# Optimization experiments

Measured on AMD Instinct MI355X. Metric: run time of the kernel, lower is better.

Reference implementation:

```python
import jax, jax.numpy as jnp
import numpy as np

EMB = 1024
HEADS = 16
HEAD_DIM = EMB // HEADS


def setup_inputs() -> dict:
    key = jax.random.key(0)
    ks = jax.random.split(key, 6)
    B, S = 4, 1024
    inputs = jax.random.normal(ks[0], (B, S, EMB), dtype=jnp.float32)
    # causal mask: 1.0 where attention is disallowed (added * -1e9 in the layer)
    mask = (1.0 - jnp.tril(jnp.ones((S, S), dtype=jnp.float32)))[None, None, :, :]
    scale = 1.0 / np.sqrt(EMB)
    wq = jax.random.normal(ks[1], (EMB, EMB), dtype=jnp.float32) * scale
    wk = jax.random.normal(ks[2], (EMB, EMB), dtype=jnp.float32) * scale
    wv = jax.random.normal(ks[3], (EMB, EMB), dtype=jnp.float32) * scale
    wo = jax.random.normal(ks[4], (EMB, EMB), dtype=jnp.float32) * scale
    zb = jnp.zeros((EMB,), dtype=jnp.float32)
    return {"inputs": inputs, "mask": mask, "wq": wq, "bq": zb, "wk": wk,
            "bk": zb, "wv": wv, "bv": zb, "wo": wo, "bo": zb}


def _split_heads(t, B):
    # [B, S, E] -> [B, H, S, Dh]
    return t.reshape(B, -1, HEADS, HEAD_DIM).transpose(0, 2, 1, 3)


def reference(inputs, mask, wq, bq, wk, bk, wv, bv, wo, bo):
    B = inputs.shape[0]
    q = _split_heads(inputs @ wq + bq, B)
    k = _split_heads(inputs @ wk + bk, B)
    v = _split_heads(inputs @ wv + bv, B)
    # NOTE: source divides by sqrt(sqrt(head_num)) = head_num**0.25
    scores = jnp.einsum('bhsd,bhtd->bhst', q, k) / jnp.asarray(HEADS, inputs.dtype) ** 0.25
    if mask is not None:
        scores = scores + mask * -1e9
    attn = jax.nn.softmax(scores, axis=-1)
    z = jnp.einsum('bhst,bhtd->bhsd', attn, v)
    # Faithful to source: reshape [B,H,S,Dh] -> [B,S,E] WITHOUT transposing heads back
    z = z.reshape(B, -1, EMB)
    return z @ wo + bo
```

## Files before the change

### kernel.cpp

```cpp
#include <hip/hip_runtime.h>
#include <hip/hip_bf16.h>
#include <stdint.h>

typedef __attribute__((ext_vector_type(8))) short short8;
typedef __attribute__((ext_vector_type(4))) float float4v;

#define SEQ   1024
#define NQKV  3072

__device__ __forceinline__ float bf2f(ushort h) {
    union { uint u; float f; } c; c.u = ((uint)h) << 16; return c.f;
}
__device__ __forceinline__ ushort f2bf(float f) {
    union { uint u; float f; } c; c.f = f;
    uint u = c.u;
    return (ushort)((u + 0x7fffu + ((u >> 16) & 1u)) >> 16);
}
__device__ __forceinline__ void gl2lds16(const ushort* g, ushort* l) {
    __builtin_amdgcn_global_load_lds(
        (const __attribute__((address_space(1))) unsigned int*)(g),
        (__attribute__((address_space(3))) unsigned int*)(l),
        16, 0, 0);
}

__global__ void detect_k(const uint* __restrict__ x, int* __restrict__ flag) {
    __shared__ int cnt[256];
    int h = 0;
    for (int i = threadIdx.x; i < 4096; i += 256) {
        uint w = x[i];
        uint e = (w >> 7) & 0xFFu;
        h += (e >= 100u && e <= 130u) ? 1 : 0;
    }
    cnt[threadIdx.x] = h;
    __syncthreads();
    if (threadIdx.x == 0) {
        int s = 0;
        for (int i = 0; i < 256; i++) s += cnt[i];
        flag[0] = (s > 2048) ? 0 : 1;
    }
}

__global__ __launch_bounds__(256) void xcvt_k(const void* __restrict__ x,
                                              ushort* __restrict__ xc,
                                              const int* __restrict__ flag) {
    int i = (blockIdx.x * 256 + threadIdx.x) * 4;
    if (*flag) {
        const float* xf = (const float*)x;
        float4 v = *(const float4*)(xf + i);
        ushort4 o;
        o.x = f2bf(v.x); o.y = f2bf(v.y); o.z = f2bf(v.z); o.w = f2bf(v.w);
        *(ushort4*)(xc + i) = o;
    } else {
        *(ushort4*)(xc + i) = *(const ushort4*)((const ushort*)x + i);
    }
}

__global__ void biascat_k(const void* __restrict__ bq, const void* __restrict__ bk,
                          const void* __restrict__ bv, const void* __restrict__ bo,
                          const int* __restrict__ flag, ushort* __restrict__ bout) {
    int i = blockIdx.x * 256 + threadIdx.x;
    int sel = i >> 10, j = i & 1023;
    const void* p = (sel == 0) ? bq : (sel == 1) ? bk : (sel == 2) ? bv : bo;
    bout[i] = (*flag) ? f2bf(((const float*)p)[j]) : ((const ushort*)p)[j];
}

__global__ __launch_bounds__(256) void transpose4_k(const void* __restrict__ w0,
                                                    const void* __restrict__ w1,
                                                    const void* __restrict__ w2,
                                                    const void* __restrict__ w3,
                                                    ushort* __restrict__ outall,
                                                    const int* __restrict__ flag) {
    __shared__ ushort tile[64][72];
    int z = blockIdx.z;
    const void* in = (z == 0) ? w0 : (z == 1) ? w1 : (z == 2) ? w2 : w3;
    ushort* out = outall + (size_t)z * 1024 * 1024;
    int k0 = blockIdx.x * 64;
    int n0 = blockIdx.y * 64;
    int t = threadIdx.x;
    int r = t >> 3, c = (t & 7) * 8;
    bool isf = (*flag != 0);
#pragma unroll
    for (int p = 0; p < 2; p++) {
        int rr = r + p * 32;
        if (isf) {
            const float* src = (const float*)in + (size_t)(k0 + rr) * 1024 + n0 + c;
            float4 v0 = *(const float4*)src;
            float4 v1 = *(const float4*)(src + 4);
            tile[rr][c + 0] = f2bf(v0.x); tile[rr][c + 1] = f2bf(v0.y);
            tile[rr][c + 2] = f2bf(v0.z); tile[rr][c + 3] = f2bf(v0.w);
            tile[rr][c + 4] = f2bf(v1.x); tile[rr][c + 5] = f2bf(v1.y);
            tile[rr][c + 6] = f2bf(v1.z); tile[rr][c + 7] = f2bf(v1.w);
        } else {
            uint4 v = *(const uint4*)((const ushort*)in + (size_t)(k0 + rr) * 1024 + n0 + c);
            *(uint4*)&tile[rr][c] = v;
        }
    }
    __syncthreads();
#pragma unroll
    for (int p = 0; p < 2; p++) {
        int n = r + p * 32;
        ushort vals[8];
#pragma unroll
        for (int j = 0; j < 8; j++) vals[j] = tile[c + j][n];
        *(uint4*)(out + (size_t)(n0 + n) * 1024 + k0 + c) = *(uint4*)vals;
    }
}

__global__ __launch_bounds__(256) void vtrans_k(const ushort* __restrict__ qkv,
                                                ushort* __restrict__ vt) {
    __shared__ ushort tile[64][72];
    int t0 = blockIdx.x * 64;
    int bh = blockIdx.y;
    int b = bh >> 4, h = bh & 15;
    int t = threadIdx.x;
    int r = t >> 3, c = (t & 7) * 8;
#pragma unroll
    for (int p = 0; p < 2; p++) {
        int rr = r + p * 32;
        uint4 v = *(const uint4*)(qkv + (size_t)(b * 1024 + t0 + rr) * NQKV + 2048 + h * 64 + c);
        *(uint4*)&tile[rr][c] = v;
    }
    __syncthreads();
#pragma unroll
    for (int p = 0; p < 2; p++) {
        int d = r + p * 32;
        ushort vals[8];
#pragma unroll
        for (int j = 0; j < 8; j++) vals[j] = tile[c + j][d];
        *(uint4*)(vt + ((size_t)bh * 64 + d) * 1024 + t0 + c) = *(uint4*)vals;
    }
}

template <bool DUAL>
__global__ __launch_bounds__(256) void gemm128_k(const ushort* __restrict__ A,
                                                 const ushort* __restrict__ BT,
                                                 const ushort* __restrict__ bias,
                                                 void* __restrict__ C,
                                                 const int* __restrict__ flag,
                                                 int M, int N, int K) {
    __shared__ ushort As[128 * 32];
    __shared__ ushort Bs[128 * 32];
    int n0 = blockIdx.x * 128, m0 = blockIdx.y * 128;
    int t = threadIdx.x;
    int w = t >> 6, lane = t & 63, q = lane >> 4, ln = lane & 15;
    int wr = w >> 1, wc = w & 1;

    float4v acc[4][4];
#pragma unroll
    for (int r = 0; r < 4; r++)
#pragma unroll
        for (int cc = 0; cc < 4; cc++) acc[r][cc] = (float4v){0.f, 0.f, 0.f, 0.f};

    for (int k0 = 0; k0 < K; k0 += 32) {
#pragma unroll
        for (int j = 0; j < 2; j++) {
            int c = j * 256 + t;
            int row = c >> 2, s = c & 3;
            int kc = s ^ ((row >> 1) & 3);
            gl2lds16(A + (size_t)(m0 + row) * K + k0 + kc * 8, &As[c * 8]);
            gl2lds16(BT + (size_t)(n0 + row) * K + k0 + kc * 8, &Bs[c * 8]);
        }
        __syncthreads();
        short8 af[4], bf[4];
#pragma unroll
        for (int r = 0; r < 4; r++) {
            int row = wr * 64 + r * 16 + ln;
            af[r] = *(const short8*)&As[((row << 2) | (q ^ ((row >> 1) & 3))) * 8];
            int col = wc * 64 + r * 16 + ln;
            bf[r] = *(const short8*)&Bs[((col << 2) | (q ^ ((col >> 1) & 3))) * 8];
        }
#pragma unroll
        for (int r = 0; r < 4; r++)
#pragma unroll
            for (int cc = 0; cc < 4; cc++)
                acc[r][cc] = __builtin_amdgcn_mfma_f32_16x16x32_bf16(af[r], bf[cc], acc[r][cc], 0, 0, 0);
        __syncthreads();
    }

    bool outf = DUAL && (*flag != 0);
#pragma unroll
    for (int cc = 0; cc < 4; cc++) {
        int n = n0 + wc * 64 + cc * 16 + ln;
        float bs = bf2f(bias[n]);
#pragma unroll
        for (int r = 0; r < 4; r++) {
#pragma unroll
            for (int i = 0; i < 4; i++) {
                int m = m0 + wr * 64 + r * 16 + q * 4 + i;
                float v = acc[r][cc][i] + bs;
                if (outf) ((float*)C)[(size_t)m * N + n] = v;
                else      ((ushort*)C)[(size_t)m * N + n] = f2bf(v);
            }
        }
    }
}

__global__ __launch_bounds__(256) void attn_k(const ushort* __restrict__ qkv,
                                              const ushort* __restrict__ vt,
                                              ushort* __restrict__ zp) {
    __shared__ ushort Ks[64 * 72];
    __shared__ ushort Vs[64 * 72];
    __shared__ ushort P[4][16 * 76];
    int pr = blockIdx.x;
    int bh = blockIdx.y;
    int b = bh >> 4, h = bh & 15;
    int t = threadIdx.x;
    int w = t >> 6, lane = t & 63, q = lane >> 4, ln = lane & 15;

    const ushort* Qp = qkv + (size_t)(b * SEQ) * NQKV + h * 64;
    const ushort* Kp = qkv + (size_t)(b * SEQ) * NQKV + 1024 + h * 64;
    const ushort* Vt = vt + (size_t)bh * 64 * 1024;

    int srr = t >> 3;
    int scol = (t & 7) * 8;

    for (int rep = 0; rep < 2; rep++) {
        int ti = rep ? (15 - pr) : pr;
        int s0 = ti * 64, sw = s0 + w * 16;

        short8 aq0 = *(const short8*)(Qp + (size_t)(sw + ln) * NQKV + q * 8);
        short8 aq1 = *(const short8*)(Qp + (size_t)(sw + ln) * NQKV + 32 + q * 8);

        float m_i[4], l_i[4];
        float4v o[4];
#pragma unroll
        for (int i = 0; i < 4; i++) { m_i[i] = -__builtin_inff(); l_i[i] = 0.f; }
#pragma unroll
        for (int nb = 0; nb < 4; nb++) o[nb] = (float4v){0.f, 0.f, 0.f, 0.f};

        for (int kt = 0; kt <= ti; kt++) {
            int t0 = kt * 64;
            __syncthreads();
#pragma unroll
            for (int p2 = 0; p2 < 2; p2++) {
                int r = srr + p2 * 32;
                *(uint4*)&Ks[r * 72 + scol] = *(const uint4*)(Kp + (size_t)(t0 + r) * NQKV + scol);
                *(uint4*)&Vs[r * 72 + scol] = *(const uint4*)(Vt + (size_t)r * 1024 + t0 + scol);
            }
            __syncthreads();

            float4v s[4];
#pragma unroll
            for (int nb = 0; nb < 4; nb++) s[nb] = (float4v){0.f, 0.f, 0.f, 0.f};
#pragma unroll
            for (int nb = 0; nb < 4; nb++) {
                short8 kf0 = *(const short8*)&Ks[(nb * 16 + ln) * 72 + q * 8];
                short8 kf1 = *(const short8*)&Ks[(nb * 16 + ln) * 72 + 32 + q * 8];
                s[nb] = __builtin_amdgcn_mfma_f32_16x16x32_bf16(aq0, kf0, s[nb], 0, 0, 0);
                s[nb] = __builtin_amdgcn_mfma_f32_16x16x32_bf16(aq1, kf1, s[nb], 0, 0, 0);
            }
            float sc[4][4];
#pragma unroll
            for (int nb = 0; nb < 4; nb++)
#pragma unroll
                for (int i = 0; i < 4; i++) {
                    int srow = sw + q * 4 + i;
                    int col = t0 + nb * 16 + ln;
                    sc[nb][i] = (col <= srow) ? s[nb][i] * 0.5f : -1e30f;
                }
            float p[4][4];
#pragma unroll
            for (int i = 0; i < 4; i++) {
                float bm = fmaxf(fmaxf(sc[0][i], sc[1][i]), fmaxf(sc[2][i], sc[3][i]));
#pragma unroll
                for (int mk = 1; mk < 16; mk <<= 1) bm = fmaxf(bm, __shfl_xor(bm, mk, 64));
                float mn = fmaxf(m_i[i], bm);
                float alpha = __expf(m_i[i] - mn);
                float sum = 0.f;
#pragma unroll
                for (int nb = 0; nb < 4; nb++) {
                    p[nb][i] = __expf(sc[nb][i] - mn);
                    sum += p[nb][i];
                }
#pragma unroll
                for (int mk = 1; mk < 16; mk <<= 1) sum += __shfl_xor(sum, mk, 64);
                l_i[i] = l_i[i] * alpha + sum;
                m_i[i] = mn;
#pragma unroll
                for (int nb = 0; nb < 4; nb++) o[nb][i] *= alpha;
            }
#pragma unroll
            for (int nb = 0; nb < 4; nb++)
#pragma unroll
                for (int i = 0; i < 4; i++)
                    P[w][(q * 4 + i) * 76 + nb * 16 + ln] = f2bf(p[nb][i]);
            asm volatile("s_waitcnt lgkmcnt(0)\n" ::: "memory");
            short8 ap0 = *(const short8*)&P[w][ln * 76 + q * 8];
            short8 ap1 = *(const short8*)&P[w][ln * 76 + 32 + q * 8];
#pragma unroll
            for (int nb = 0; nb < 4; nb++) {
                short8 bv0 = *(const short8*)&Vs[(nb * 16 + ln) * 72 + q * 8];
                short8 bv1 = *(const short8*)&Vs[(nb * 16 + ln) * 72 + 32 + q * 8];
                o[nb] = __builtin_amdgcn_mfma_f32_16x16x32_bf16(ap0, bv0, o[nb], 0, 0, 0);
                o[nb] = __builtin_amdgcn_mfma_f32_16x16x32_bf16(ap1, bv1, o[nb], 0, 0, 0);
            }
        }

#pragma unroll
        for (int nb = 0; nb < 4; nb++) {
#pragma unroll
            for (int i = 0; i < 4; i++) {
                int srow = sw + q * 4 + i;
                int d = nb * 16 + ln;
                float z = o[nb][i] / l_i[i];
                int sp = h * 64 + (srow >> 4);
                int ep = ((srow & 15) << 6) + d;
                zp[((size_t)(b * SEQ + sp)) * 1024 + ep] = f2bf(z);
            }
        }
    }
}

extern "C" void kernel_launch(void* const* d_in, const int* in_sizes, int n_in,
                              void* d_out, int out_size, void* d_ws, size_t ws_size,
                              hipStream_t stream) {
    const void* X  = d_in[0];
    const void* wq = d_in[2];
    const void* bq = d_in[3];
    const void* wk = d_in[4];
    const void* bk = d_in[5];
    const void* wv = d_in[6];
    const void* bv = d_in[7];
    const void* wo = d_in[8];
    const void* bo = d_in[9];

    char* ws = (char*)d_ws;
    int*    flag  = (int*)ws;
    ushort* biasq = (ushort*)(ws + 4096);
    ushort* WTall = (ushort*)(ws + 12288);
    ushort* Xc    = (ushort*)(ws + 8400896);
    ushort* QKV   = (ushort*)(ws + 16789504);
    ushort* VT    = (ushort*)(ws + 41955328);
    ushort* WTo   = WTall + 3 * 1024 * 1024;
    ushort* ZP    = Xc;

    detect_k<<<1, 256, 0, stream>>>((const uint*)X, flag);
    xcvt_k<<<4096, 256, 0, stream>>>(X, Xc, flag);
    biascat_k<<<16, 256, 0, stream>>>(bq, bk, bv, bo, flag, biasq);
    transpose4_k<<<dim3(16, 16, 4), 256, 0, stream>>>(wq, wk, wv, wo, WTall, flag);
    gemm128_k<false><<<dim3(24, 32), 256, 0, stream>>>(Xc, WTall, biasq, QKV, flag, 4096, NQKV, 1024);
    vtrans_k<<<dim3(16, 64), 256, 0, stream>>>(QKV, VT);
    attn_k<<<dim3(8, 64), 256, 0, stream>>>(QKV, VT, ZP);
    gemm128_k<true><<<dim3(8, 32), 256, 0, stream>>>(ZP, WTo, biasq + 3072, d_out, flag, 4096, 1024, 1024);
}
```

Measured before the change: 214.2 us.

## Use direct global-to-LDS loads with XOR swizzle and one query tile per block

The attention kernel now stages K and V tiles with global_load_lds 16-byte direct copies into an XOR-swizzled unpadded LDS layout, instead of loading into registers and then storing to padded LDS. The paired-tile loop (pr and 15-pr) is removed: each block handles one query tile, with heaviest tiles launched first, which doubles the grid. The causal mask is applied only on the diagonal tile. These target register staging cost, LDS bank conflicts and per-block work imbalance, at the cost of losing the balanced pairing and relying on the runtime to schedule the uneven blocks.

```diff
diff --git a/kernel.cpp b/kernel.cpp
--- a/kernel.cpp
+++ b/kernel.cpp
@@ -198,58 +198,61 @@
 __global__ __launch_bounds__(256) void attn_k(const ushort* __restrict__ qkv,
                                               const ushort* __restrict__ vt,
                                               ushort* __restrict__ zp) {
-    __shared__ ushort Ks[64 * 72];
-    __shared__ ushort Vs[64 * 72];
+    __shared__ ushort Ks[64 * 64];
+    __shared__ ushort Vs[64 * 64];
     __shared__ ushort P[4][16 * 76];
-    int pr = blockIdx.x;
+    int ti = 15 - blockIdx.x;
     int bh = blockIdx.y;
     int b = bh >> 4, h = bh & 15;
     int t = threadIdx.x;
     int w = t >> 6, lane = t & 63, q = lane >> 4, ln = lane & 15;
+    int sw = ti * 64 + w * 16;
 
     const ushort* Qp = qkv + (size_t)(b * SEQ) * NQKV + h * 64;
     const ushort* Kp = qkv + (size_t)(b * SEQ) * NQKV + 1024 + h * 64;
     const ushort* Vt = vt + (size_t)bh * 64 * 1024;
 
-    int srr = t >> 3;
-    int scol = (t & 7) * 8;
-
-    for (int rep = 0; rep < 2; rep++) {
-        int ti = rep ? (15 - pr) : pr;
-        int s0 = ti * 64, sw = s0 + w * 16;
-
-        short8 aq0 = *(const short8*)(Qp + (size_t)(sw + ln) * NQKV + q * 8);
-        short8 aq1 = *(const short8*)(Qp + (size_t)(sw + ln) * NQKV + 32 + q * 8);
-
-        float m_i[4], l_i[4];
-        float4v o[4];
-#pragma unroll
-        for (int i = 0; i < 4; i++) { m_i[i] = -__builtin_inff(); l_i[i] = 0.f; }
-#pragma unroll
-        for (int nb = 0; nb < 4; nb++) o[nb] = (float4v){0.f, 0.f, 0.f, 0.f};
-
-        for (int kt = 0; kt <= ti; kt++) {
-            int t0 = kt * 64;
-            __syncthreads();
-#pragma unroll
-            for (int p2 = 0; p2 < 2; p2++) {
-                int r = srr + p2 * 32;
-                *(uint4*)&Ks[r * 72 + scol] = *(const uint4*)(Kp + (size_t)(t0 + r) * NQKV + scol);
-                *(uint4*)&Vs[r * 72 + scol] = *(const uint4*)(Vt + (size_t)r * 1024 + t0 + scol);
-            }
-            __syncthreads();
-
-            float4v s[4];
-#pragma unroll
-            for (int nb = 0; nb < 4; nb++) s[nb] = (float4v){0.f, 0.f, 0.f, 0.f};
-#pragma unroll
-            for (int nb = 0; nb < 4; nb++) {
-                short8 kf0 = *(const short8*)&Ks[(nb * 16 + ln) * 72 + q * 8];
-                short8 kf1 = *(const short8*)&Ks[(nb * 16 + ln) * 72 + 32 + q * 8];
-                s[nb] = __builtin_amdgcn_mfma_f32_16x16x32_bf16(aq0, kf0, s[nb], 0, 0, 0);
-                s[nb] = __builtin_amdgcn_mfma_f32_16x16x32_bf16(aq1, kf1, s[nb], 0, 0, 0);
-            }
-            float sc[4][4];
+    short8 aq0 = *(const short8*)(Qp + (size_t)(sw + ln) * NQKV + q * 8);
+    short8 aq1 = *(const short8*)(Qp + (size_t)(sw + ln) * NQKV + 32 + q * 8);
+
+    float m_i[4], l_i[4];
+    float4v o[4];
+#pragma unroll
+    for (int i = 0; i < 4; i++) { m_i[i] = -__builtin_inff(); l_i[i] = 0.f; }
+#pragma unroll
+    for (int nb = 0; nb < 4; nb++) o[nb] = (float4v){0.f, 0.f, 0.f, 0.f};
+
+    int rA = ln;
+    for (int kt = 0; kt <= ti; kt++) {
+        int t0 = kt * 64;
+        __syncthreads();
+#pragma unroll
+        for (int j = 0; j < 2; j++) {
+            int c = j * 256 + t;
+            int row = c >> 3, s = c & 7;
+            int kc = s ^ (row & 7);
+            gl2lds16(Kp + (size_t)(t0 + row) * NQKV + kc * 8, &Ks[c * 8]);
+            gl2lds16(Vt + (size_t)row * 1024 + t0 + kc * 8, &Vs[c * 8]);
+        }
+        __syncthreads();
+
+        float4v s[4];
+#pragma unroll
+        for (int nb = 0; nb < 4; nb++) {
+            int row = nb * 16 + rA;
+            short8 kf0 = *(const short8*)&Ks[((row << 3) | (q ^ (row & 7))) * 8];
+            short8 kf1 = *(const short8*)&Ks[((row << 3) | ((4 + q) ^ (row & 7))) * 8];
+            s[nb] = (float4v){0.f, 0.f, 0.f, 0.f};
+            s[nb] = __builtin_amdgcn_mfma_f32_16x16x32_bf16(aq0, kf0, s[nb], 0, 0, 0);
+            s[nb] = __builtin_amdgcn_mfma_f32_16x16x32_bf16(aq1, kf1, s[nb], 0, 0, 0);
+        }
+        float sc[4][4];
+        if (kt < ti) {
+#pragma unroll
+            for (int nb = 0; nb < 4; nb++)
+#pragma unroll
+                for (int i = 0; i < 4; i++) sc[nb][i] = s[nb][i] * 0.5f;
+        } else {
 #pragma unroll
             for (int nb = 0; nb < 4; nb++)
 #pragma unroll
@@ -258,55 +261,56 @@
                     int col = t0 + nb * 16 + ln;
                     sc[nb][i] = (col <= srow) ? s[nb][i] * 0.5f : -1e30f;
                 }
-            float p[4][4];
-#pragma unroll
-            for (int i = 0; i < 4; i++) {
-                float bm = fmaxf(fmaxf(sc[0][i], sc[1][i]), fmaxf(sc[2][i], sc[3][i]));
-#pragma unroll
-                for (int mk = 1; mk < 16; mk <<= 1) bm = fmaxf(bm, __shfl_xor(bm, mk, 64));
-                float mn = fmaxf(m_i[i], bm);
-                float alpha = __expf(m_i[i] - mn);
-                float sum = 0.f;
-#pragma unroll
-                for (int nb = 0; nb < 4; nb++) {
-                    p[nb][i] = __expf(sc[nb][i] - mn);
-                    sum += p[nb][i];
-                }
-#pragma unroll
-                for (int mk = 1; mk < 16; mk <<= 1) sum += __shfl_xor(sum, mk, 64);
-                l_i[i] = l_i[i] * alpha + sum;
-                m_i[i] = mn;
-#pragma unroll
-                for (int nb = 0; nb < 4; nb++) o[nb][i] *= alpha;
+        }
+        float p[4][4];
+#pragma unroll
+        for (int i = 0; i < 4; i++) {
+            float bm = fmaxf(fmaxf(sc[0][i], sc[1][i]), fmaxf(sc[2][i], sc[3][i]));
+#pragma unroll
+            for (int mk = 1; mk < 16; mk <<= 1) bm = fmaxf(bm, __shfl_xor(bm, mk, 64));
+            float mn = fmaxf(m_i[i], bm);
+            float alpha = __expf(m_i[i] - mn);
+            float sum = 0.f;
+#pragma unroll
+            for (int nb = 0; nb < 4; nb++) {
+                p[nb][i] = __expf(sc[nb][i] - mn);
+                sum += p[nb][i];
             }
 #pragma unroll
-            for (int nb = 0; nb < 4; nb++)
-#pragma unroll
-                for (int i = 0; i < 4; i++)
-                    P[w][(q * 4 + i) * 76 + nb * 16 + ln] = f2bf(p[nb][i]);
-            asm volatile("s_waitcnt lgkmcnt(0)\n" ::: "memory");
-            short8 ap0 = *(const short8*)&P[w][ln * 76 + q * 8];
-            short8 ap1 = *(const short8*)&P[w][ln * 76 + 32 + q * 8];
-#pragma unroll
-            for (int nb = 0; nb < 4; nb++) {
-                short8 bv0 = *(const short8*)&Vs[(nb * 16 + ln) * 72 + q * 8];
-                short8 bv1 = *(const short8*)&Vs[(nb * 16 + ln) * 72 + 32 + q * 8];
-                o[nb] = __builtin_amdgcn_mfma_f32_16x16x32_bf16(ap0, bv0, o[nb], 0, 0, 0);
-                o[nb] = __builtin_amdgcn_mfma_f32_16x16x32_bf16(ap1, bv1, o[nb], 0, 0, 0);
-            }
-        }
-
+            for (int mk = 1; mk < 16; mk <<= 1) sum += __shfl_xor(sum, mk, 64);
+            l_i[i] = l_i[i] * alpha + sum;
+            m_i[i] = mn;
+#pragma unroll
+            for (int nb = 0; nb < 4; nb++) o[nb][i] *= alpha;
+        }
+#pragma unroll
+        for (int nb = 0; nb < 4; nb++)
+#pragma unroll
+            for (int i = 0; i < 4; i++)
+                P[w][(q * 4 + i) * 76 + nb * 16 + ln] = f2bf(p[nb][i]);
+        asm volatile("s_waitcnt lgkmcnt(0)\n" ::: "memory");
+        short8 ap0 = *(const short8*)&P[w][ln * 76 + q * 8];
+        short8 ap1 = *(const short8*)&P[w][ln * 76 + 32 + q * 8];
 #pragma unroll
         for (int nb = 0; nb < 4; nb++) {
-#pragma unroll
-            for (int i = 0; i < 4; i++) {
-                int srow = sw + q * 4 + i;
-                int d = nb * 16 + ln;
-                float z = o[nb][i] / l_i[i];
-                int sp = h * 64 + (srow >> 4);
-                int ep = ((srow & 15) << 6) + d;
-                zp[((size_t)(b * SEQ + sp)) * 1024 + ep] = f2bf(z);
-            }
+            int row = nb * 16 + rA;
+            short8 bv0 = *(const short8*)&Vs[((row << 3) | (q ^ (row & 7))) * 8];
+            short8 bv1 = *(const short8*)&Vs[((row << 3) | ((4 + q) ^ (row & 7))) * 8];
+            o[nb] = __builtin_amdgcn_mfma_f32_16x16x32_bf16(ap0, bv0, o[nb], 0, 0, 0);
+            o[nb] = __builtin_amdgcn_mfma_f32_16x16x32_bf16(ap1, bv1, o[nb], 0, 0, 0);
+        }
+    }
+
+#pragma unroll
+    for (int nb = 0; nb < 4; nb++) {
+#pragma unroll
+        for (int i = 0; i < 4; i++) {
+            int srow = sw + q * 4 + i;
+            int d = nb * 16 + ln;
+            float z = o[nb][i] / l_i[i];
+            int sp = h * 64 + (srow >> 4);
+            int ep = ((srow & 15) << 6) + d;
+            zp[((size_t)(b * SEQ + sp)) * 1024 + ep] = f2bf(z);
         }
     }
 }
@@ -340,6 +344,6 @@
     transpose4_k<<<dim3(16, 16, 4), 256, 0, stream>>>(wq, wk, wv, wo, WTall, flag);
     gemm128_k<false><<<dim3(24, 32), 256, 0, stream>>>(Xc, WTall, biasq, QKV, flag, 4096, NQKV, 1024);
     vtrans_k<<<dim3(16, 64), 256, 0, stream>>>(QKV, VT);
-    attn_k<<<dim3(8, 64), 256, 0, stream>>>(QKV, VT, ZP);
+    attn_k<<<dim3(16, 64), 256, 0, stream>>>(QKV, VT, ZP);
     gemm128_k<true><<<dim3(8, 32), 256, 0, stream>>>(ZP, WTo, biasq + 3072, d_out, flag, 4096, 1024, 1024);
 }
```

New measurement: 229.4 us. 1.07x slower.

## Double-buffer attention K/V tiles with async global-to-LDS loads and XOR swizzle

Applied to the files above, without the earlier changes.

The attention kernel now stages K and V tiles into two LDS buffers using direct global-to-LDS loads. The next tile is prefetched while the current one is consumed, replacing the synchronous load-store-barrier sequence. The LDS layout drops row padding in favour of an XOR swizzle on 16-byte chunks to avoid bank conflicts. The causal mask is now applied only on the diagonal tile. This costs twice the K/V LDS footprint and depends on the barrier draining outstanding async loads before a buffer is read.

```diff
diff --git a/kernel.cpp b/kernel.cpp
--- a/kernel.cpp
+++ b/kernel.cpp
@@ -198,8 +198,8 @@
 __global__ __launch_bounds__(256) void attn_k(const ushort* __restrict__ qkv,
                                               const ushort* __restrict__ vt,
                                               ushort* __restrict__ zp) {
-    __shared__ ushort Ks[64 * 72];
-    __shared__ ushort Vs[64 * 72];
+    __shared__ ushort Ks[2][64 * 64];
+    __shared__ ushort Vs[2][64 * 64];
     __shared__ ushort P[4][16 * 76];
     int pr = blockIdx.x;
     int bh = blockIdx.y;
@@ -211,12 +211,15 @@
     const ushort* Kp = qkv + (size_t)(b * SEQ) * NQKV + 1024 + h * 64;
     const ushort* Vt = vt + (size_t)bh * 64 * 1024;
 
-    int srr = t >> 3;
-    int scol = (t & 7) * 8;
+    int c0 = t, c1 = 256 + t;
+    int row0 = c0 >> 3, kc0 = (c0 & 7) ^ (row0 & 7);
+    int row1 = c1 >> 3, kc1 = (c1 & 7) ^ (row1 & 7);
 
     for (int rep = 0; rep < 2; rep++) {
         int ti = rep ? (15 - pr) : pr;
-        int s0 = ti * 64, sw = s0 + w * 16;
+        int sw = ti * 64 + w * 16;
+
+        __syncthreads();
 
         short8 aq0 = *(const short8*)(Qp + (size_t)(sw + ln) * NQKV + q * 8);
         short8 aq1 = *(const short8*)(Qp + (size_t)(sw + ln) * NQKV + 32 + q * 8);
@@ -228,36 +231,49 @@
 #pragma unroll
         for (int nb = 0; nb < 4; nb++) o[nb] = (float4v){0.f, 0.f, 0.f, 0.f};
 
+        gl2lds16(Kp + (size_t)row0 * NQKV + kc0 * 8, &Ks[0][c0 * 8]);
+        gl2lds16(Vt + (size_t)row0 * 1024 + kc0 * 8, &Vs[0][c0 * 8]);
+        gl2lds16(Kp + (size_t)row1 * NQKV + kc1 * 8, &Ks[0][c1 * 8]);
+        gl2lds16(Vt + (size_t)row1 * 1024 + kc1 * 8, &Vs[0][c1 * 8]);
+
         for (int kt = 0; kt <= ti; kt++) {
+            int cur = kt & 1;
             int t0 = kt * 64;
             __syncthreads();
-#pragma unroll
-            for (int p2 = 0; p2 < 2; p2++) {
-                int r = srr + p2 * 32;
-                *(uint4*)&Ks[r * 72 + scol] = *(const uint4*)(Kp + (size_t)(t0 + r) * NQKV + scol);
-                *(uint4*)&Vs[r * 72 + scol] = *(const uint4*)(Vt + (size_t)r * 1024 + t0 + scol);
-            }
-            __syncthreads();
+            if (kt < ti) {
+                int nt0 = t0 + 64, nxt = cur ^ 1;
+                gl2lds16(Kp + (size_t)(nt0 + row0) * NQKV + kc0 * 8, &Ks[nxt][c0 * 8]);
+                gl2lds16(Vt + (size_t)row0 * 1024 + nt0 + kc0 * 8, &Vs[nxt][c0 * 8]);
+                gl2lds16(Kp + (size_t)(nt0 + row1) * NQKV + kc1 * 8, &Ks[nxt][c1 * 8]);
+                gl2lds16(Vt + (size_t)row1 * 1024 + nt0 + kc1 * 8, &Vs[nxt][c1 * 8]);
+            }
 
             float4v s[4];
 #pragma unroll
-            for (int nb = 0; nb < 4; nb++) s[nb] = (float4v){0.f, 0.f, 0.f, 0.f};
-#pragma unroll
             for (int nb = 0; nb < 4; nb++) {
-                short8 kf0 = *(const short8*)&Ks[(nb * 16 + ln) * 72 + q * 8];
-                short8 kf1 = *(const short8*)&Ks[(nb * 16 + ln) * 72 + 32 + q * 8];
+                int row = nb * 16 + ln;
+                short8 kf0 = *(const short8*)&Ks[cur][((row << 3) | (q ^ (row & 7))) * 8];
+                short8 kf1 = *(const short8*)&Ks[cur][((row << 3) | ((4 + q) ^ (row & 7))) * 8];
+                s[nb] = (float4v){0.f, 0.f, 0.f, 0.f};
                 s[nb] = __builtin_amdgcn_mfma_f32_16x16x32_bf16(aq0, kf0, s[nb], 0, 0, 0);
                 s[nb] = __builtin_amdgcn_mfma_f32_16x16x32_bf16(aq1, kf1, s[nb], 0, 0, 0);
             }
             float sc[4][4];
-#pragma unroll
-            for (int nb = 0; nb < 4; nb++)
-#pragma unroll
-                for (int i = 0; i < 4; i++) {
-                    int srow = sw + q * 4 + i;
-                    int col = t0 + nb * 16 + ln;
-                    sc[nb][i] = (col <= srow) ? s[nb][i] * 0.5f : -1e30f;
-                }
+            if (kt < ti) {
+#pragma unroll
+                for (int nb = 0; nb < 4; nb++)
+#pragma unroll
+                    for (int i = 0; i < 4; i++) sc[nb][i] = s[nb][i] * 0.5f;
+            } else {
+#pragma unroll
+                for (int nb = 0; nb < 4; nb++)
+#pragma unroll
+                    for (int i = 0; i < 4; i++) {
+                        int srow = sw + q * 4 + i;
+                        int col = t0 + nb * 16 + ln;
+                        sc[nb][i] = (col <= srow) ? s[nb][i] * 0.5f : -1e30f;
+                    }
+            }
             float p[4][4];
 #pragma unroll
             for (int i = 0; i < 4; i++) {
@@ -289,8 +305,9 @@
             short8 ap1 = *(const short8*)&P[w][ln * 76 + 32 + q * 8];
 #pragma unroll
             for (int nb = 0; nb < 4; nb++) {
-                short8 bv0 = *(const short8*)&Vs[(nb * 16 + ln) * 72 + q * 8];
-                short8 bv1 = *(const short8*)&Vs[(nb * 16 + ln) * 72 + 32 + q * 8];
+                int row = nb * 16 + ln;
+                short8 bv0 = *(const short8*)&Vs[cur][((row << 3) | (q ^ (row & 7))) * 8];
+                short8 bv1 = *(const short8*)&Vs[cur][((row << 3) | ((4 + q) ^ (row & 7))) * 8];
                 o[nb] = __builtin_amdgcn_mfma_f32_16x16x32_bf16(ap0, bv0, o[nb], 0, 0, 0);
                 o[nb] = __builtin_amdgcn_mfma_f32_16x16x32_bf16(ap1, bv1, o[nb], 0, 0, 0);
             }
```

New measurement: 213.7 us. Within noise of the previous version (-0.2%).
